# Kernel optimization log

Hardware: AMD Instinct MI355X
Metric: run time of the kernel (lower is better)

## Reference

```python
import jax, jax.numpy as jnp
import numpy as np

CHUNK = 64  # chunk_size
EPS = 1e-6


def setup_inputs() -> dict:
    key = jax.random.key(0)
    ks = jax.random.split(key, 7)
    b, L, H, dh, ds = 2, 4096, 16, 64, 64
    X = jax.random.normal(ks[0], (b, L, H, dh), dtype=jnp.float32)
    # negative log-decay in (-1, 0) for numerical stability (Mamba2 convention)
    A = -jax.random.uniform(ks[1], (b, L, H), dtype=jnp.float32)
    B = jax.random.normal(ks[2], (b, L, H, ds), dtype=jnp.float32)
    C = jax.random.normal(ks[3], (b, L, H, ds), dtype=jnp.float32)
    log2_alpha_base = jnp.full((H,), -0.15, dtype=jnp.float32) + 0.02 * jax.random.normal(ks[4], (H,), dtype=jnp.float32)
    log2_beta = 0.02 * jax.random.normal(ks[5], (H,), dtype=jnp.float32)
    surprise_ema = jnp.ones((H,), dtype=jnp.float32)
    return {"X": X, "A": A, "B": B, "C": C,
            "log2_alpha_base": log2_alpha_base, "log2_beta": log2_beta,
            "surprise_ema": surprise_ema}


def reference(X, A, B, C, log2_alpha_base, log2_beta, surprise_ema):
    b, L, H, dh = X.shape
    ds = B.shape[-1]
    n = L // CHUNK  # L is a multiple of CHUNK (no padding needed)

    # [b, h, n, c, ...] layout
    Xt = X.reshape(b, n, CHUNK, H, dh).transpose(0, 3, 1, 2, 4)   # b h n c dh
    At = A.reshape(b, n, CHUNK, H).transpose(0, 3, 1, 2)          # b h n c
    Bt = B.reshape(b, n, CHUNK, H, ds).transpose(0, 3, 1, 2, 4)   # b h n c ds
    Ct = C.reshape(b, n, CHUNK, H, ds).transpose(0, 3, 1, 2, 4)   # b h n c ds

    # per-chunk surprise from outer-product state delta
    BX = jnp.einsum('bhncs,bhncd->bhnsd', Bt, Xt)                 # b h n ds dh
    chunk_surprise = (BX ** 2).mean(axis=(-1, -2))                # b h n

    # surprise gate (eval mode: EMA buffer not updated)
    normalized = chunk_surprise / (surprise_ema[None, :, None] + EPS)
    log2c = jnp.clip(log2_alpha_base, -3.32, -0.015)
    alpha_base = 1.0 - jnp.exp2(log2c)                            # [H]
    beta = jnp.exp2(jnp.clip(log2_beta, -2.0, 2.0))               # [H]
    boost = jax.nn.relu(jnp.tanh(beta[None, :, None] * normalized))
    alpha = jnp.clip(alpha_base[None, :, None]
                     + (1.0 - alpha_base[None, :, None]) * boost, 0.01, 0.999)

    # surprise-modulated decay
    A_mod = At * (1.0 - alpha)[..., None]                         # b h n c
    A_cs = jnp.cumsum(A_mod, axis=-1)                             # b h n c

    # intra-chunk attention-like term with causal decay matrix
    diff = A_cs[..., :, None] - A_cs[..., None, :]                # b h n c c
    causal = jnp.tril(jnp.ones((CHUNK, CHUNK), dtype=bool))
    Lmat = jnp.where(causal, jnp.exp(diff), 0.0)
    CB = jnp.einsum('bhnid,bhnjd->bhnij', Ct, Bt)
    Y_intra = jnp.einsum('bhnij,bhnjd->bhnid', Lmat * CB, Xt)

    # inter-chunk state carry (sequential over chunks)
    decay_chunk = jnp.exp(A_mod.sum(axis=-1))                     # b h n
    decay_to_end = jnp.exp(A_cs[..., -1:] - A_cs)                 # b h n c
    h_final = jnp.einsum('bhnc,bhncs,bhncd->bhnsd', decay_to_end, Bt, Xt)

    def step(carry, inp):
        dc, hf = inp                                              # dc: b h ; hf: b h ds dh
        return dc[..., None, None] * carry + hf, carry

    dc_n = jnp.moveaxis(decay_chunk, 2, 0)                        # n b h
    hf_n = jnp.moveaxis(h_final, 2, 0)                            # n b h ds dh
    init = jnp.zeros((b, H, ds, dh), X.dtype)
    _, h_inter_n = jax.lax.scan(step, init, (dc_n, hf_n))
    h_inter = jnp.moveaxis(h_inter_n, 0, 2)                       # b h n ds dh

    decay_from_start = jnp.exp(A_cs)
    Y_inter = jnp.einsum('bhnis,bhnsp,bhni->bhnip', Ct, h_inter, decay_from_start)

    Y = (Y_intra + Y_inter).transpose(0, 2, 3, 1, 4).reshape(b, L, H, dh)
    return Y
```

## Files before the change

kernel.cpp:

```cpp
#include <hip/hip_runtime.h>
#include <hip/hip_bf16.h>
#include <math.h>

#define LSEQ 4096
#define NH   16
#define DH   64
#define CH   64
#define NCH  64
#define LDT  72

typedef __attribute__((ext_vector_type(8))) short bf16x8;
typedef __attribute__((ext_vector_type(4))) short s16x4;
typedef __attribute__((ext_vector_type(4))) float f32x4;

#define MFMA16(a, b, c) __builtin_amdgcn_mfma_f32_16x16x32_bf16((a), (b), (c), 0, 0, 0)

__device__ __forceinline__ float4 ld4(const float* p) {
    return *reinterpret_cast<const float4*>(p);
}
__device__ __forceinline__ short f2b(float x) {
    __hip_bfloat16 h = __float2bfloat16(x);
    return *reinterpret_cast<short*>(&h);
}
__device__ __forceinline__ float b2f(short s) {
    union { unsigned u; float f; } v;
    v.u = ((unsigned)(unsigned short)s) << 16;
    return v.f;
}
__device__ __forceinline__ s16x4 pack4(float a, float b, float c, float d) {
    s16x4 r; r.x = f2b(a); r.y = f2b(b); r.z = f2b(c); r.w = f2b(d); return r;
}

__global__ __launch_bounds__(256) void ssd_k1(
    const float* __restrict__ X, const float* __restrict__ A,
    const float* __restrict__ B, const float* __restrict__ C,
    const float* __restrict__ l2ab, const float* __restrict__ l2b,
    const float* __restrict__ ema,
    unsigned short* __restrict__ yw, unsigned short* __restrict__ hf,
    float* __restrict__ dcb, float* __restrict__ dfs)
{
    __shared__ __align__(16) short sXT[CH * LDT];
    __shared__ __align__(16) short sBT[CH * LDT];
    __shared__ __align__(16) short sB [CH * LDT];
    __shared__ __align__(16) short sC [CH * LDT];
    __shared__ float sA[CH], sAcs[CH], sDte[CH], sEp[CH], sEn[CH], red[4];

    const int tid  = threadIdx.x;
    const int blk  = blockIdx.x;
    const int nidx = blk & (NCH - 1);
    const int h    = (blk >> 6) & (NH - 1);
    const int bb   = blk >> 10;
    const size_t base = ((size_t)(bb * LSEQ + nidx * CH) * NH + h) * DH;

    #pragma unroll
    for (int m = 0; m < 4; ++m) {
        int p = tid + 256 * m;
        int c = p >> 4, q = p & 15, d0 = q * 4;
        size_t g = base + (size_t)c * 1024 + d0;
        float4 xv = ld4(&X[g]);
        float4 bv = ld4(&B[g]);
        float4 cv = ld4(&C[g]);
        *reinterpret_cast<s16x4*>(&sC[c * LDT + d0]) = pack4(cv.x, cv.y, cv.z, cv.w);
        *reinterpret_cast<s16x4*>(&sB[c * LDT + d0]) = pack4(bv.x, bv.y, bv.z, bv.w);
        float xf[4] = {xv.x, xv.y, xv.z, xv.w};
        float bf[4] = {bv.x, bv.y, bv.z, bv.w};
        #pragma unroll
        for (int ee = 0; ee < 4; ++ee) {
            int e = (ee + q) & 3;
            sXT[(d0 + e) * LDT + c] = f2b(xf[e]);
            sBT[(d0 + e) * LDT + c] = f2b(bf[e]);
        }
    }
    if (tid < CH) sA[tid] = A[(size_t)(bb * LSEQ + nidx * CH + tid) * NH + h];
    __syncthreads();

    const int lane = tid & 63;
    const int w    = tid >> 6;
    const int rb   = 16 * w;
    const int fr   = lane & 15;
    const int g4   = 4 * (lane >> 4);
    const int ko   = 8 * (lane >> 4);
    const f32x4 zf = {0.f, 0.f, 0.f, 0.f};

    f32x4 acc0[4] = {zf, zf, zf, zf};
    #pragma unroll
    for (int k0 = 0; k0 < 64; k0 += 32) {
        bf16x8 a = *reinterpret_cast<const bf16x8*>(&sBT[(rb + fr) * LDT + k0 + ko]);
        #pragma unroll
        for (int n = 0; n < 4; ++n) {
            bf16x8 b = *reinterpret_cast<const bf16x8*>(&sXT[(16 * n + fr) * LDT + k0 + ko]);
            acc0[n] = MFMA16(a, b, acc0[n]);
        }
    }
    float ss = 0.f;
    #pragma unroll
    for (int n = 0; n < 4; ++n)
        #pragma unroll
        for (int r = 0; r < 4; ++r) ss += acc0[n][r] * acc0[n][r];
    #pragma unroll
    for (int off = 32; off > 0; off >>= 1) ss += __shfl_down(ss, off, 64);
    if (lane == 0) red[w] = ss;
    __syncthreads();

    if (tid < CH) {
        float surprise = (red[0] + red[1] + red[2] + red[3]) * (1.f / 4096.f);
        float l2c   = fminf(fmaxf(l2ab[h], -3.32f), -0.015f);
        float ab_   = 1.f - exp2f(l2c);
        float bt    = exp2f(fminf(fmaxf(l2b[h], -2.f), 2.f));
        float nrm   = surprise / (ema[h] + 1e-6f);
        float boost = fmaxf(tanhf(bt * nrm), 0.f);
        float alpha = fminf(fmaxf(ab_ + (1.f - ab_) * boost, 0.01f), 0.999f);
        float scale = 1.f - alpha;
        float v = sA[tid] * scale;
        #pragma unroll
        for (int off = 1; off < 64; off <<= 1) {
            float t = __shfl_up(v, off, 64);
            if (tid >= off) v += t;
        }
        float tot = __shfl(v, 63, 64);
        float ep  = expf(v);
        sAcs[tid] = v;
        sEp[tid]  = ep;
        sEn[tid]  = expf(-v);
        sDte[tid] = expf(tot - v);
        dfs[(size_t)blk * CH + tid] = ep;
        if (tid == 63) dcb[blk] = expf(tot);
    }
    __syncthreads();

    #pragma unroll
    for (int m = 0; m < 4; ++m) {
        int p = tid + 256 * m;
        int s = p >> 4, c0 = 4 * (p & 15);
        s16x4 v = *reinterpret_cast<s16x4*>(&sBT[s * LDT + c0]);
        v.x = f2b(b2f(v.x) * sDte[c0]);
        v.y = f2b(b2f(v.y) * sDte[c0 + 1]);
        v.z = f2b(b2f(v.z) * sDte[c0 + 2]);
        v.w = f2b(b2f(v.w) * sDte[c0 + 3]);
        *reinterpret_cast<s16x4*>(&sBT[s * LDT + c0]) = v;
    }

    f32x4 acc1[4] = {zf, zf, zf, zf};
    #pragma unroll
    for (int k0 = 0; k0 < 64; k0 += 32) {
        bf16x8 a = *reinterpret_cast<const bf16x8*>(&sC[(rb + fr) * LDT + k0 + ko]);
        #pragma unroll
        for (int n = 0; n < 4; ++n) {
            bf16x8 b = *reinterpret_cast<const bf16x8*>(&sB[(16 * n + fr) * LDT + k0 + ko]);
            acc1[n] = MFMA16(a, b, acc1[n]);
        }
    }
    __syncthreads();

    short* sT = sB;
    #pragma unroll
    for (int n = 0; n < 4; ++n)
        #pragma unroll
        for (int r = 0; r < 4; ++r) {
            int i = rb + g4 + r;
            int j = 16 * n + fr;
            float val = (j <= i) ? sEp[i] * sEn[j] * acc1[n][r] : 0.f;
            sT[i * LDT + j] = f2b(val);
        }
    __syncthreads();

    f32x4 acc2[4] = {zf, zf, zf, zf};
    f32x4 acc3[4] = {zf, zf, zf, zf};
    #pragma unroll
    for (int k0 = 0; k0 < 64; k0 += 32) {
        bf16x8 aX = *reinterpret_cast<const bf16x8*>(&sXT[(rb + fr) * LDT + k0 + ko]);
        bf16x8 aB = *reinterpret_cast<const bf16x8*>(&sBT[(rb + fr) * LDT + k0 + ko]);
        #pragma unroll
        for (int n = 0; n < 4; ++n) {
            bf16x8 bT = *reinterpret_cast<const bf16x8*>(&sT [(16 * n + fr) * LDT + k0 + ko]);
            bf16x8 bX = *reinterpret_cast<const bf16x8*>(&sXT[(16 * n + fr) * LDT + k0 + ko]);
            acc2[n] = MFMA16(aX, bT, acc2[n]);
            acc3[n] = MFMA16(aB, bX, acc3[n]);
        }
    }
    #pragma unroll
    for (int n = 0; n < 4; ++n) {
        int colI = 16 * n + fr;
        s16x4 y4 = pack4(acc2[n][0], acc2[n][1], acc2[n][2], acc2[n][3]);
        s16x4 h4 = pack4(acc3[n][0], acc3[n][1], acc3[n][2], acc3[n][3]);
        *reinterpret_cast<s16x4*>(&yw[(size_t)blk * 4096 + colI * 64 + rb + g4]) = y4;
        *reinterpret_cast<s16x4*>(&hf[(size_t)blk * 4096 + colI * 64 + rb + g4]) = h4;
    }
}

__global__ __launch_bounds__(256) void ssd_k2(
    unsigned int* __restrict__ hfU, const float* __restrict__ dcb)
{
    __shared__ float sdc[NCH];
    const int tid = threadIdx.x;
    const int bh  = blockIdx.x >> 3;
    const int sub = blockIdx.x & 7;
    if (tid < NCH) sdc[tid] = dcb[bh * NCH + tid];
    __syncthreads();
    const size_t base = (size_t)bh * NCH * 2048 + sub * 256 + tid;

    float c0 = 0.f, c1 = 0.f;
    unsigned int cur[8];
    #pragma unroll
    for (int kk = 0; kk < 8; ++kk) cur[kk] = hfU[base + (size_t)kk * 2048];
    #pragma unroll
    for (int kb = 0; kb < 8; ++kb) {
        unsigned int nxt[8];
        if (kb < 7) {
            #pragma unroll
            for (int kk = 0; kk < 8; ++kk)
                nxt[kk] = hfU[base + (size_t)(8 * kb + 8 + kk) * 2048];
        }
        #pragma unroll
        for (int kk = 0; kk < 8; ++kk) {
            int k = 8 * kb + kk;
            unsigned int u = cur[kk];
            union { unsigned int q; float f; } lo, hi;
            lo.q = u << 16;
            hi.q = u & 0xffff0000u;
            unsigned int packed = (unsigned int)(unsigned short)f2b(c0)
                                | ((unsigned int)(unsigned short)f2b(c1) << 16);
            hfU[base + (size_t)k * 2048] = packed;
            float d = sdc[k];
            c0 = fmaf(d, c0, lo.f);
            c1 = fmaf(d, c1, hi.f);
        }
        if (kb < 7) {
            #pragma unroll
            for (int kk = 0; kk < 8; ++kk) cur[kk] = nxt[kk];
        }
    }
}

__global__ __launch_bounds__(256) void ssd_k3(
    const float* __restrict__ C, const unsigned short* __restrict__ hI,
    const unsigned short* __restrict__ yw, const float* __restrict__ dfs,
    float* __restrict__ Y)
{
    __shared__ __align__(16) short sHt[CH * LDT];
    __shared__ __align__(16) short sC2[CH * LDT];
    __shared__ float sF[CH];

    const int tid  = threadIdx.x;
    const int blk  = blockIdx.x;
    const int nidx = blk & (NCH - 1);
    const int h    = (blk >> 6) & (NH - 1);
    const int bb   = blk >> 10;
    const size_t base = ((size_t)(bb * LSEQ + nidx * CH) * NH + h) * DH;

    #pragma unroll
    for (int m = 0; m < 2; ++m) {
        int idx = tid + 256 * m;
        int row = idx >> 3, c8 = (idx & 7) * 8;
        bf16x8 v = *reinterpret_cast<const bf16x8*>(&hI[(size_t)blk * 4096 + row * 64 + c8]);
        *reinterpret_cast<bf16x8*>(&sHt[row * LDT + c8]) = v;
    }
    #pragma unroll
    for (int m = 0; m < 4; ++m) {
        int p = tid + 256 * m;
        int row = p >> 4, d0 = (p & 15) * 4;
        float4 cv = ld4(&C[base + (size_t)row * 1024 + d0]);
        *reinterpret_cast<s16x4*>(&sC2[row * LDT + d0]) = pack4(cv.x, cv.y, cv.z, cv.w);
    }
    if (tid < CH) sF[tid] = dfs[(size_t)blk * CH + tid];
    __syncthreads();

    const int lane = tid & 63;
    const int w    = tid >> 6;
    const int rb   = 16 * w;
    const int fr   = lane & 15;
    const int g4   = 4 * (lane >> 4);
    const int ko   = 8 * (lane >> 4);
    const f32x4 zf = {0.f, 0.f, 0.f, 0.f};

    f32x4 acc[4] = {zf, zf, zf, zf};
    #pragma unroll
    for (int k0 = 0; k0 < 64; k0 += 32) {
        bf16x8 a = *reinterpret_cast<const bf16x8*>(&sHt[(rb + fr) * LDT + k0 + ko]);
        #pragma unroll
        for (int n = 0; n < 4; ++n) {
            bf16x8 b = *reinterpret_cast<const bf16x8*>(&sC2[(16 * n + fr) * LDT + k0 + ko]);
            acc[n] = MFMA16(a, b, acc[n]);
        }
    }
    #pragma unroll
    for (int n = 0; n < 4; ++n) {
        int i  = 16 * n + fr;
        int p0 = rb + g4;
        float f = sF[i];
        const unsigned short* ywp = &yw[(size_t)blk * 4096 + i * 64 + p0];
        float4 o;
        o.x = fmaf(f, acc[n][0], b2f((short)ywp[0]));
        o.y = fmaf(f, acc[n][1], b2f((short)ywp[1]));
        o.z = fmaf(f, acc[n][2], b2f((short)ywp[2]));
        o.w = fmaf(f, acc[n][3], b2f((short)ywp[3]));
        *reinterpret_cast<float4*>(&Y[base + (size_t)i * 1024 + p0]) = o;
    }
}

extern "C" void kernel_launch(void* const* d_in, const int* in_sizes, int n_in,
                              void* d_out, int out_size, void* d_ws, size_t ws_size,
                              hipStream_t stream)
{
    const float* X    = (const float*)d_in[0];
    const float* A    = (const float*)d_in[1];
    const float* B    = (const float*)d_in[2];
    const float* C    = (const float*)d_in[3];
    const float* l2ab = (const float*)d_in[4];
    const float* l2b  = (const float*)d_in[5];
    const float* ema  = (const float*)d_in[6];
    float* Y = (float*)d_out;

    unsigned short* hf = (unsigned short*)d_ws;
    unsigned short* yw = hf + (size_t)8388608;
    float* dcb = (float*)(yw + (size_t)8388608);
    float* dfs = dcb + 2048;

    const int nblk = 2 * NH * NCH;
    ssd_k1<<<nblk, 256, 0, stream>>>(X, A, B, C, l2ab, l2b, ema, yw, hf, dcb, dfs);
    ssd_k2<<<256, 256, 0, stream>>>((unsigned int*)hf, dcb);
    ssd_k3<<<nblk, 256, 0, stream>>>(C, hf, yw, dfs, Y);
}
```

Measured before the change: 62.28 us.

## Compute surprise via Gram matrices and transpose tiles with lane shuffles

Replaces the B^T X product for the surprise term with the identity sum((B^T X)^2) = <X X^T, B B^T>, so X, B and C stay in row-major LDS and the three MFMA products share one pass. The transposed X and B tiles for the final matmuls are built by cross-lane shuffles and written once after the gate. Decay exponentials are kept in registers and broadcast with shuffles, which removes the shared scalar arrays and some barriers. The change adds extra MFMAs and shuffle work, and uses the faster __expf.

```diff
diff --git a/kernel.cpp b/kernel.cpp
--- a/kernel.cpp
+++ b/kernel.cpp
@@ -29,6 +29,16 @@
 }
 __device__ __forceinline__ s16x4 pack4(float a, float b, float c, float d) {
     s16x4 r; r.x = f2b(a); r.y = f2b(b); r.z = f2b(c); r.w = f2b(d); return r;
+}
+__device__ __forceinline__ uint2 sx2(uint2 v, int m) {
+    uint2 r;
+    r.x = (unsigned)__shfl_xor((int)v.x, m, 64);
+    r.y = (unsigned)__shfl_xor((int)v.y, m, 64);
+    return r;
+}
+__device__ __forceinline__ short ext4(uint2 u, int g) {
+    unsigned word = (g & 2) ? u.y : u.x;
+    return (short)((g & 1) ? (word >> 16) : (word & 0xffffu));
 }
 
 __global__ __launch_bounds__(256) void ssd_k1(
@@ -39,11 +49,10 @@
     unsigned short* __restrict__ yw, unsigned short* __restrict__ hf,
     float* __restrict__ dcb, float* __restrict__ dfs)
 {
-    __shared__ __align__(16) short sXT[CH * LDT];
-    __shared__ __align__(16) short sBT[CH * LDT];
-    __shared__ __align__(16) short sB [CH * LDT];
-    __shared__ __align__(16) short sC [CH * LDT];
-    __shared__ float sA[CH], sAcs[CH], sDte[CH], sEp[CH], sEn[CH], red[4];
+    __shared__ __align__(16) short R1[CH * LDT];
+    __shared__ __align__(16) short R2[CH * LDT];
+    __shared__ __align__(16) short R3[CH * LDT];
+    __shared__ __align__(16) float red[4];
 
     const int tid  = threadIdx.x;
     const int blk  = blockIdx.x;
@@ -52,128 +61,146 @@
     const int bb   = blk >> 10;
     const size_t base = ((size_t)(bb * LSEQ + nidx * CH) * NH + h) * DH;
 
+    const int lane = tid & 63;
+    const int w    = tid >> 6;
+    const int rb   = 16 * w;
+    const int fr   = lane & 15;
+    const int gq   = lane >> 4;
+    const int g4   = 4 * gq;
+    const int ko   = 8 * gq;
+
     #pragma unroll
     for (int m = 0; m < 4; ++m) {
         int p = tid + 256 * m;
-        int c = p >> 4, q = p & 15, d0 = q * 4;
+        int c = p >> 4, d0 = (p & 15) * 4;
         size_t g = base + (size_t)c * 1024 + d0;
         float4 xv = ld4(&X[g]);
         float4 bv = ld4(&B[g]);
         float4 cv = ld4(&C[g]);
-        *reinterpret_cast<s16x4*>(&sC[c * LDT + d0]) = pack4(cv.x, cv.y, cv.z, cv.w);
-        *reinterpret_cast<s16x4*>(&sB[c * LDT + d0]) = pack4(bv.x, bv.y, bv.z, bv.w);
-        float xf[4] = {xv.x, xv.y, xv.z, xv.w};
-        float bf[4] = {bv.x, bv.y, bv.z, bv.w};
-        #pragma unroll
-        for (int ee = 0; ee < 4; ++ee) {
-            int e = (ee + q) & 3;
-            sXT[(d0 + e) * LDT + c] = f2b(xf[e]);
-            sBT[(d0 + e) * LDT + c] = f2b(bf[e]);
-        }
-    }
-    if (tid < CH) sA[tid] = A[(size_t)(bb * LSEQ + nidx * CH + tid) * NH + h];
-    __syncthreads();
-
-    const int lane = tid & 63;
-    const int w    = tid >> 6;
-    const int rb   = 16 * w;
-    const int fr   = lane & 15;
-    const int g4   = 4 * (lane >> 4);
-    const int ko   = 8 * (lane >> 4);
+        *reinterpret_cast<s16x4*>(&R1[c * LDT + d0]) = pack4(xv.x, xv.y, xv.z, xv.w);
+        *reinterpret_cast<s16x4*>(&R2[c * LDT + d0]) = pack4(bv.x, bv.y, bv.z, bv.w);
+        *reinterpret_cast<s16x4*>(&R3[c * LDT + d0]) = pack4(cv.x, cv.y, cv.z, cv.w);
+    }
+    float aval = A[(size_t)(bb * LSEQ + nidx * CH + lane) * NH + h];
+    __syncthreads();
+
     const f32x4 zf = {0.f, 0.f, 0.f, 0.f};
 
-    f32x4 acc0[4] = {zf, zf, zf, zf};
+    f32x4 aGX[4] = {zf, zf, zf, zf};
+    f32x4 aGB[4] = {zf, zf, zf, zf};
+    f32x4 aCB[4] = {zf, zf, zf, zf};
     #pragma unroll
     for (int k0 = 0; k0 < 64; k0 += 32) {
-        bf16x8 a = *reinterpret_cast<const bf16x8*>(&sBT[(rb + fr) * LDT + k0 + ko]);
+        bf16x8 aX = *reinterpret_cast<const bf16x8*>(&R1[(rb + fr) * LDT + k0 + ko]);
+        bf16x8 aB = *reinterpret_cast<const bf16x8*>(&R2[(rb + fr) * LDT + k0 + ko]);
+        bf16x8 aC = *reinterpret_cast<const bf16x8*>(&R3[(rb + fr) * LDT + k0 + ko]);
         #pragma unroll
         for (int n = 0; n < 4; ++n) {
-            bf16x8 b = *reinterpret_cast<const bf16x8*>(&sXT[(16 * n + fr) * LDT + k0 + ko]);
-            acc0[n] = MFMA16(a, b, acc0[n]);
+            bf16x8 bX = *reinterpret_cast<const bf16x8*>(&R1[(16 * n + fr) * LDT + k0 + ko]);
+            bf16x8 bB = *reinterpret_cast<const bf16x8*>(&R2[(16 * n + fr) * LDT + k0 + ko]);
+            aGX[n] = MFMA16(aX, bX, aGX[n]);
+            aGB[n] = MFMA16(aB, bB, aGB[n]);
+            aCB[n] = MFMA16(aC, bB, aCB[n]);
         }
     }
     float ss = 0.f;
     #pragma unroll
     for (int n = 0; n < 4; ++n)
         #pragma unroll
-        for (int r = 0; r < 4; ++r) ss += acc0[n][r] * acc0[n][r];
+        for (int r = 0; r < 4; ++r) ss += aGX[n][r] * aGB[n][r];
     #pragma unroll
     for (int off = 32; off > 0; off >>= 1) ss += __shfl_down(ss, off, 64);
     if (lane == 0) red[w] = ss;
     __syncthreads();
 
-    if (tid < CH) {
-        float surprise = (red[0] + red[1] + red[2] + red[3]) * (1.f / 4096.f);
-        float l2c   = fminf(fmaxf(l2ab[h], -3.32f), -0.015f);
-        float ab_   = 1.f - exp2f(l2c);
-        float bt    = exp2f(fminf(fmaxf(l2b[h], -2.f), 2.f));
-        float nrm   = surprise / (ema[h] + 1e-6f);
-        float boost = fmaxf(tanhf(bt * nrm), 0.f);
-        float alpha = fminf(fmaxf(ab_ + (1.f - ab_) * boost, 0.01f), 0.999f);
-        float scale = 1.f - alpha;
-        float v = sA[tid] * scale;
-        #pragma unroll
-        for (int off = 1; off < 64; off <<= 1) {
-            float t = __shfl_up(v, off, 64);
-            if (tid >= off) v += t;
-        }
-        float tot = __shfl(v, 63, 64);
-        float ep  = expf(v);
-        sAcs[tid] = v;
-        sEp[tid]  = ep;
-        sEn[tid]  = expf(-v);
-        sDte[tid] = expf(tot - v);
-        dfs[(size_t)blk * CH + tid] = ep;
-        if (tid == 63) dcb[blk] = expf(tot);
-    }
-    __syncthreads();
-
+    float4 rv = *reinterpret_cast<const float4*>(red);
+    float surprise = (rv.x + rv.y + rv.z + rv.w) * (1.f / 4096.f);
+    float l2c   = fminf(fmaxf(l2ab[h], -3.32f), -0.015f);
+    float ab_   = 1.f - exp2f(l2c);
+    float bt    = exp2f(fminf(fmaxf(l2b[h], -2.f), 2.f));
+    float nrm   = surprise / (ema[h] + 1e-6f);
+    float boost = fmaxf(tanhf(bt * nrm), 0.f);
+    float alpha = fminf(fmaxf(ab_ + (1.f - ab_) * boost, 0.01f), 0.999f);
+    float scale = 1.f - alpha;
+    float v = aval * scale;
+    #pragma unroll
+    for (int off = 1; off < 64; off <<= 1) {
+        float t = __shfl_up(v, off, 64);
+        if (lane >= off) v += t;
+    }
+    float tot  = __shfl(v, 63, 64);
+    float epv  = __expf(v);
+    float env  = __expf(-v);
+    float dtev = __expf(tot - v);
+    if (w == 0) {
+        dfs[(size_t)blk * CH + lane] = epv;
+        if (lane == 63) dcb[blk] = __expf(tot);
+    }
+
+    {
+        float epi[4], enj[4];
+        #pragma unroll
+        for (int r = 0; r < 4; ++r) epi[r] = __shfl(epv, rb + g4 + r, 64);
+        #pragma unroll
+        for (int n = 0; n < 4; ++n) enj[n] = __shfl(env, 16 * n + fr, 64);
+        #pragma unroll
+        for (int n = 0; n < 4; ++n)
+            #pragma unroll
+            for (int r = 0; r < 4; ++r) {
+                int i = rb + g4 + r, j = 16 * n + fr;
+                float val = (j <= i) ? epi[r] * enj[n] * aCB[n][r] : 0.f;
+                R3[i * LDT + j] = f2b(val);
+            }
+    }
+
+    s16x4 outX[4], outB[4];
+    const int d0 = 4 * fr;
     #pragma unroll
     for (int m = 0; m < 4; ++m) {
-        int p = tid + 256 * m;
-        int s = p >> 4, c0 = 4 * (p & 15);
-        s16x4 v = *reinterpret_cast<s16x4*>(&sBT[s * LDT + c0]);
-        v.x = f2b(b2f(v.x) * sDte[c0]);
-        v.y = f2b(b2f(v.y) * sDte[c0 + 1]);
-        v.z = f2b(b2f(v.z) * sDte[c0 + 2]);
-        v.w = f2b(b2f(v.w) * sDte[c0 + 3]);
-        *reinterpret_cast<s16x4*>(&sBT[s * LDT + c0]) = v;
-    }
-
-    f32x4 acc1[4] = {zf, zf, zf, zf};
-    #pragma unroll
-    for (int k0 = 0; k0 < 64; k0 += 32) {
-        bf16x8 a = *reinterpret_cast<const bf16x8*>(&sC[(rb + fr) * LDT + k0 + ko]);
-        #pragma unroll
-        for (int n = 0; n < 4; ++n) {
-            bf16x8 b = *reinterpret_cast<const bf16x8*>(&sB[(16 * n + fr) * LDT + k0 + ko]);
-            acc1[n] = MFMA16(a, b, acc1[n]);
-        }
-    }
-    __syncthreads();
-
-    short* sT = sB;
-    #pragma unroll
-    for (int n = 0; n < 4; ++n)
-        #pragma unroll
-        for (int r = 0; r < 4; ++r) {
-            int i = rb + g4 + r;
-            int j = 16 * n + fr;
-            float val = (j <= i) ? sEp[i] * sEn[j] * acc1[n][r] : 0.f;
-            sT[i * LDT + j] = f2b(val);
-        }
+        int c0 = 16 * w + 4 * m;
+        uint2 mx = *reinterpret_cast<const uint2*>(&R1[(c0 + gq) * LDT + d0]);
+        uint2 mb = *reinterpret_cast<const uint2*>(&R2[(c0 + gq) * LDT + d0]);
+        uint2 px = sx2(mx, 16), pb = sx2(mb, 16);
+        uint2 xe = (gq & 1) ? px : mx, xo = (gq & 1) ? mx : px;
+        uint2 be = (gq & 1) ? pb : mb, bo = (gq & 1) ? mb : pb;
+        uint2 xpe = sx2(xe, 32), xpo = sx2(xo, 32);
+        uint2 bpe = sx2(be, 32), bpo = sx2(bo, 32);
+        uint2 xr0 = (gq & 2) ? xpe : xe, xr1 = (gq & 2) ? xpo : xo;
+        uint2 xr2 = (gq & 2) ? xe : xpe, xr3 = (gq & 2) ? xo : xpo;
+        uint2 br0 = (gq & 2) ? bpe : be, br1 = (gq & 2) ? bpo : bo;
+        uint2 br2 = (gq & 2) ? be : bpe, br3 = (gq & 2) ? bo : bpo;
+        s16x4 ox; ox.x = ext4(xr0, gq); ox.y = ext4(xr1, gq);
+                  ox.z = ext4(xr2, gq); ox.w = ext4(xr3, gq);
+        outX[m] = ox;
+        float dt0 = __shfl(dtev, c0 + 0, 64), dt1 = __shfl(dtev, c0 + 1, 64);
+        float dt2 = __shfl(dtev, c0 + 2, 64), dt3 = __shfl(dtev, c0 + 3, 64);
+        s16x4 ob;
+        ob.x = f2b(b2f(ext4(br0, gq)) * dt0);
+        ob.y = f2b(b2f(ext4(br1, gq)) * dt1);
+        ob.z = f2b(b2f(ext4(br2, gq)) * dt2);
+        ob.w = f2b(b2f(ext4(br3, gq)) * dt3);
+        outB[m] = ob;
+    }
+    __syncthreads();
+
+    #pragma unroll
+    for (int m = 0; m < 4; ++m) {
+        int c0 = 16 * w + 4 * m;
+        *reinterpret_cast<s16x4*>(&R1[(d0 + gq) * LDT + c0]) = outX[m];
+        *reinterpret_cast<s16x4*>(&R2[(d0 + gq) * LDT + c0]) = outB[m];
+    }
     __syncthreads();
 
     f32x4 acc2[4] = {zf, zf, zf, zf};
     f32x4 acc3[4] = {zf, zf, zf, zf};
     #pragma unroll
     for (int k0 = 0; k0 < 64; k0 += 32) {
-        bf16x8 aX = *reinterpret_cast<const bf16x8*>(&sXT[(rb + fr) * LDT + k0 + ko]);
-        bf16x8 aB = *reinterpret_cast<const bf16x8*>(&sBT[(rb + fr) * LDT + k0 + ko]);
+        bf16x8 aX = *reinterpret_cast<const bf16x8*>(&R1[(rb + fr) * LDT + k0 + ko]);
+        bf16x8 aB = *reinterpret_cast<const bf16x8*>(&R2[(rb + fr) * LDT + k0 + ko]);
         #pragma unroll
         for (int n = 0; n < 4; ++n) {
-            bf16x8 bT = *reinterpret_cast<const bf16x8*>(&sT [(16 * n + fr) * LDT + k0 + ko]);
-            bf16x8 bX = *reinterpret_cast<const bf16x8*>(&sXT[(16 * n + fr) * LDT + k0 + ko]);
+            bf16x8 bT = *reinterpret_cast<const bf16x8*>(&R3[(16 * n + fr) * LDT + k0 + ko]);
+            bf16x8 bX = *reinterpret_cast<const bf16x8*>(&R1[(16 * n + fr) * LDT + k0 + ko]);
             acc2[n] = MFMA16(aX, bT, acc2[n]);
             acc3[n] = MFMA16(aB, bX, acc3[n]);
         }
```

Measured after the change: 57.97 us. 6.9% less time.
